# Performance work log

Hardware: AMD Instinct MI355X
Metric: run time of the kernel (lower is better)

Reference implementation:

```python
import jax, jax.numpy as jnp
import numpy as np


def setup_inputs() -> dict:
    key = jax.random.key(0)
    ks = jax.random.split(key, 8)
    C = 128
    Cq = C // 8  # 16
    x = jax.random.normal(ks[0], (4, C, 64, 64), dtype=jnp.float32)
    s = 1.0 / np.sqrt(C)
    wq = jax.random.normal(ks[1], (Cq, C), dtype=jnp.float32) * s
    bq = jnp.zeros((Cq,), dtype=jnp.float32)
    wk = jax.random.normal(ks[2], (Cq, C), dtype=jnp.float32) * s
    bk = jnp.zeros((Cq,), dtype=jnp.float32)
    wv = jax.random.normal(ks[3], (C, C), dtype=jnp.float32) * s
    bv = jnp.zeros((C,), dtype=jnp.float32)
    gamma = jnp.array([0.5], dtype=jnp.float32)
    return {"x": x, "wq": wq, "bq": bq, "wk": wk, "bk": bk,
            "wv": wv, "bv": bv, "gamma": gamma}


def reference(x, wq, bq, wk, bk, wv, bv, gamma):
    B, C, W, H = x.shape
    N = W * H
    xf = x.reshape(B, C, N)  # flatten spatial; 1x1 conv == channel matmul
    q = jnp.einsum('qc,bcn->bnq', wq, xf) + bq[None, None, :]  # B,N,Cq
    k = jnp.einsum('qc,bcn->bqn', wk, xf) + bk[None, :, None]  # B,Cq,N
    v = jnp.einsum('vc,bcn->bvn', wv, xf) + bv[None, :, None]  # B,C,N
    energy = jnp.einsum('bnq,bqm->bnm', q, k)                  # B,N,N (no scaling)
    attention = jax.nn.softmax(energy, axis=-1)
    out = jnp.einsum('bvm,bnm->bvn', v, attention)             # V @ A^T
    out = out.reshape(B, C, W, H)
    return gamma[0] * out + x
```

## Files before the change

### kernel.cpp

```cpp
#include <hip/hip_runtime.h>

#define B_    4
#define C_    128
#define CQ_   16
#define N_    4096
#define KVBLK 64

typedef short          s16x8 __attribute__((ext_vector_type(8)));
typedef unsigned short u16x4 __attribute__((ext_vector_type(4)));
typedef unsigned int   u32x4 __attribute__((ext_vector_type(4)));
typedef float          f32x4 __attribute__((ext_vector_type(4)));
typedef unsigned short u16;
typedef unsigned int   u32;

__device__ __forceinline__ u16 f2bf(float f) {
    unsigned int u = __builtin_bit_cast(unsigned int, f);
    u += 0x7fffu + ((u >> 16) & 1u);
    return (u16)(u >> 16);
}
__device__ __forceinline__ float bf2f(u16 h) {
    unsigned int u = ((unsigned int)h) << 16;
    return __builtin_bit_cast(float, u);
}
__device__ __forceinline__ s16x8 ld8bf(const u16* p) {
    return *reinterpret_cast<const s16x8*>(p);
}
__device__ __forceinline__ u32 cvtpk_bf16(float lo, float hi) {
    u32 r;
    asm("v_cvt_pk_bf16_f32 %0, %1, %2" : "=v"(r) : "v"(lo), "v"(hi));
    return r;
}
__device__ __forceinline__ void gld_lds16(const u16* src, u16* lds) {
    __builtin_amdgcn_global_load_lds(
        (const __attribute__((address_space(1))) void*)src,
        (__attribute__((address_space(3))) void*)lds, 16, 0, 0);
}

__global__ __launch_bounds__(256) void proj_all_kernel(
    const float* __restrict__ x,
    const float* __restrict__ wq, const float* __restrict__ bq,
    const float* __restrict__ wk, const float* __restrict__ bk,
    const float* __restrict__ wv, const float* __restrict__ bv,
    u16* __restrict__ Qb, u16* __restrict__ Kb, u16* __restrict__ Vb)
{
    __shared__ float smem[12800];
    const int tid = threadIdx.x;
    const int b   = blockIdx.y;
    const int nl  = tid & 63;
    const int n   = blockIdx.x * 64 + nl;
    const int ch  = tid >> 6;
    const float* xp = x + ((size_t)b * C_) * N_ + n;

    if (blockIdx.z == 0) {
        float* wqs = smem;
        float* wks = smem + 2048;
        float (*part)[4][64][17] = (float (*)[4][64][17])(smem + 4096);
        for (int i = tid; i < CQ_ * C_; i += 256) { wqs[i] = wq[i]; wks[i] = wk[i]; }
        __syncthreads();

        float qa[CQ_], ka[CQ_];
#pragma unroll
        for (int j = 0; j < CQ_; ++j) { qa[j] = 0.f; ka[j] = 0.f; }
        const int c0 = ch * 32;
        for (int c = c0; c < c0 + 32; ++c) {
            const float xv = xp[(size_t)c * N_];
#pragma unroll
            for (int j = 0; j < CQ_; ++j) {
                qa[j] = fmaf(wqs[j * C_ + c], xv, qa[j]);
                ka[j] = fmaf(wks[j * C_ + c], xv, ka[j]);
            }
        }
#pragma unroll
        for (int j = 0; j < CQ_; ++j) { part[0][ch][nl][j] = qa[j]; part[1][ch][nl][j] = ka[j]; }
        __syncthreads();

        if (tid < 128) {
            const int which = tid >> 6;
            const int n2 = tid & 63;
            const float* bias = which ? bk : bq;
            alignas(16) u16 row[32];
#pragma unroll
            for (int j = 0; j < CQ_; ++j) {
                float v = part[which][0][n2][j] + part[which][1][n2][j]
                        + part[which][2][n2][j] + part[which][3][n2][j] + bias[j];
                u16 h = f2bf(v);
                row[j]       = h;
                row[CQ_ + j] = f2bf(v - bf2f(h));
            }
            u16* dst = (which ? Kb : Qb) + ((size_t)(b * N_ + blockIdx.x * 64 + n2)) * 32;
#pragma unroll
            for (int i = 0; i < 4; ++i)
                reinterpret_cast<uint4*>(dst)[i] = reinterpret_cast<const uint4*>(row)[i];
        }
    } else {
        const int cv0 = (blockIdx.z - 1) * 32;
        float* wvs = smem;
        float (*part)[64][33] = (float (*)[64][33])(smem + 4096);
        for (int i = tid; i < 32 * C_; i += 256) wvs[i] = wv[cv0 * C_ + i];
        __syncthreads();

        float acc[32];
#pragma unroll
        for (int j = 0; j < 32; ++j) acc[j] = 0.f;
        const int c0 = ch * 32;
        for (int c = c0; c < c0 + 32; ++c) {
            const float xv = xp[(size_t)c * N_];
#pragma unroll
            for (int j = 0; j < 32; ++j) acc[j] = fmaf(wvs[j * C_ + c], xv, acc[j]);
        }
#pragma unroll
        for (int j = 0; j < 32; ++j) part[ch][nl][j] = acc[j];
        __syncthreads();

        const int jq = tid >> 6;
#pragma unroll
        for (int jj = 0; jj < 8; ++jj) {
            const int j = jq * 8 + jj;
            float v = part[0][nl][j] + part[1][nl][j] + part[2][nl][j] + part[3][nl][j]
                    + bv[cv0 + j];
            Vb[((size_t)(b * C_ + cv0 + j)) * N_ + blockIdx.x * 64 + nl] = f2bf(v);
        }
    }
}

template<int NSPLIT>
__global__ __launch_bounds__(256, 2) void attn_split_kernel(
    const u16* __restrict__ Qb, const u16* __restrict__ Kb, const u16* __restrict__ Vb,
    u16* __restrict__ Opart, float* __restrict__ Lpart)
{
    constexpr int MPER = N_ / NSPLIT;
    constexpr int NT   = MPER / KVBLK;

    __shared__ __align__(16) u16 Kt[2][KVBLK * 32];
    __shared__ __align__(16) u16 Vt[2][C_ * KVBLK];

    const int tid  = threadIdx.x;
    const int lane = tid & 63;
    const int l16  = lane & 15;
    const int g    = lane >> 4;
    const int wave = tid >> 6;
    const int b    = blockIdx.y;
    const int n0   = blockIdx.x * 128;
    const int s    = blockIdx.z;
    const int ms   = s * MPER;

    const int qn = n0 + wave * 32 + l16;
    const s16x8 qf0 = ld8bf(Qb + ((size_t)(b * N_ + qn)) * 32 + 8 * g);
    const s16x8 qf1 = ld8bf(Qb + ((size_t)(b * N_ + qn + 16)) * 32 + 8 * g);

    const int kv_s   = tid >> 2;
    const int kcol_s = ((tid & 3) * 16) ^ ((kv_s & 3) << 4);
    const u16* ksrc0 = Kb + ((size_t)b * N_ + kv_s) * 32 + (kcol_s >> 1);
    const int vc_s   = tid >> 3;
    const u16* vsrc0[4];
#pragma unroll
    for (int i = 0; i < 4; ++i) {
        const int c_i  = i * 32 + vc_s;
        const int vcol = ((tid & 7) * 16) ^ ((c_i & 7) << 4);
        vsrc0[i] = Vb + ((size_t)(b * C_ + c_i)) * N_ + (vcol >> 1);
    }

    const int kswz  = (l16 & 3) << 4;
    const int vswz  = (l16 & 7) << 4;
    const int koff1 = l16 * 32 + (((16 * (g & 1)) ^ kswz) >> 1);
    const int koff2 = l16 * 32 + (((32 + 16 * g) ^ kswz) >> 1);
    const int voffA = l16 * 64 + (((16 * g) ^ vswz) >> 1);
    const int voffB = l16 * 64 + (((64 + 16 * g) ^ vswz) >> 1);

    const bool hig = (g >= 2);
    const bool mid = (g == 1) || (g == 2);

    f32x4 acc0[8], acc1[8];
#pragma unroll
    for (int cg = 0; cg < 8; ++cg) { acc0[cg] = {}; acc1[cg] = {}; }
    float lp0 = 0.f, lp1 = 0.f;

    auto relayout = [&](const float (&p)[4][4], int ss) -> s16x8 {
        const u32 a0 = cvtpk_bf16(p[2 * ss][0],     p[2 * ss][1]);
        const u32 b0 = cvtpk_bf16(p[2 * ss][2],     p[2 * ss][3]);
        const u32 a1 = cvtpk_bf16(p[2 * ss + 1][0], p[2 * ss + 1][1]);
        const u32 b1 = cvtpk_bf16(p[2 * ss + 1][2], p[2 * ss + 1][3]);
        const u32 mA = (u32)__shfl_xor((int)(hig ? a0 : a1), 32);
        const u32 mB = (u32)__shfl_xor((int)(hig ? b0 : b1), 32);
        const u32 oA = hig ? a1 : a0;
        const u32 oB = hig ? b1 : b0;
        const u32 eA = mid ? mA : oA;
        const u32 eB = mid ? mB : oB;
        const u32 vA = mid ? oA : mA;
        const u32 vB = mid ? oB : mB;
        const u32 xA = (u32)__shfl_xor((int)vA, 16);
        const u32 xB = (u32)__shfl_xor((int)vB, 16);
        u32x4 w;
        w[0] = (g & 1) ? xA : eA;
        w[1] = (g & 1) ? xB : eB;
        w[2] = (g & 1) ? eA : xA;
        w[3] = (g & 1) ? eB : xB;
        return __builtin_bit_cast(s16x8, w);
    };

    auto body = [&](int t, int buf) {
        if (t + 1 < NT) {
            const int mn = ms + (t + 1) * KVBLK;
            gld_lds16(ksrc0 + (size_t)mn * 32, &Kt[buf ^ 1][wave * 512]);
#pragma unroll
            for (int i = 0; i < 4; ++i)
                gld_lds16(vsrc0[i] + mn, &Vt[buf ^ 1][i * 2048 + wave * 512]);
        }
        const u16* ktb = &Kt[buf][0];
        const u16* vtb = &Vt[buf][0];

        f32x4 s0[4], s1[4];
        __builtin_amdgcn_s_setprio(1);
#pragma unroll
        for (int mg = 0; mg < 4; ++mg) {
            const s16x8 kf1 = ld8bf(ktb + koff1 + mg * 512);
            s16x8 kf2 = {};
            if (g < 2) kf2 = ld8bf(ktb + koff2 + mg * 512);
            f32x4 z0 = {}, z1 = {};
            z0 = __builtin_amdgcn_mfma_f32_16x16x32_bf16(kf1, qf0, z0, 0, 0, 0);
            z0 = __builtin_amdgcn_mfma_f32_16x16x32_bf16(kf2, qf0, z0, 0, 0, 0);
            z1 = __builtin_amdgcn_mfma_f32_16x16x32_bf16(kf1, qf1, z1, 0, 0, 0);
            z1 = __builtin_amdgcn_mfma_f32_16x16x32_bf16(kf2, qf1, z1, 0, 0, 0);
            s0[mg] = z0; s1[mg] = z1;
        }
        __builtin_amdgcn_s_setprio(0);

        s16x8 pf00, pf01, pf10, pf11;
        {
            float p[4][4];
#pragma unroll
            for (int mg = 0; mg < 4; ++mg)
#pragma unroll
                for (int i = 0; i < 4; ++i) { p[mg][i] = __expf(s0[mg][i]); lp0 += p[mg][i]; }
            pf00 = relayout(p, 0); pf01 = relayout(p, 1);
        }
        {
            float p[4][4];
#pragma unroll
            for (int mg = 0; mg < 4; ++mg)
#pragma unroll
                for (int i = 0; i < 4; ++i) { p[mg][i] = __expf(s1[mg][i]); lp1 += p[mg][i]; }
            pf10 = relayout(p, 0); pf11 = relayout(p, 1);
        }

        __builtin_amdgcn_s_setprio(1);
#pragma unroll
        for (int cg = 0; cg < 8; ++cg) {
            const s16x8 vfa = ld8bf(vtb + voffA + cg * 1024);
            acc0[cg] = __builtin_amdgcn_mfma_f32_16x16x32_bf16(vfa, pf00, acc0[cg], 0, 0, 0);
            acc1[cg] = __builtin_amdgcn_mfma_f32_16x16x32_bf16(vfa, pf10, acc1[cg], 0, 0, 0);
            const s16x8 vfb = ld8bf(vtb + voffB + cg * 1024);
            acc0[cg] = __builtin_amdgcn_mfma_f32_16x16x32_bf16(vfb, pf01, acc0[cg], 0, 0, 0);
            acc1[cg] = __builtin_amdgcn_mfma_f32_16x16x32_bf16(vfb, pf11, acc1[cg], 0, 0, 0);
        }
        __builtin_amdgcn_s_setprio(0);

        asm volatile("s_waitcnt vmcnt(0)" ::: "memory");
        __syncthreads();
    };

    gld_lds16(ksrc0 + (size_t)ms * 32, &Kt[0][wave * 512]);
#pragma unroll
    for (int i = 0; i < 4; ++i)
        gld_lds16(vsrc0[i] + ms, &Vt[0][i * 2048 + wave * 512]);
    asm volatile("s_waitcnt vmcnt(0)" ::: "memory");
    __syncthreads();

    for (int tt = 0; tt < NT / 2; ++tt) {
        body(2 * tt, 0);
        body(2 * tt + 1, 1);
    }

    lp0 += __shfl_xor(lp0, 16);  lp0 += __shfl_xor(lp0, 32);
    lp1 += __shfl_xor(lp1, 16);  lp1 += __shfl_xor(lp1, 32);
    const size_t sb = (size_t)(s * B_ + b);
    if (lane < 16) {
        Lpart[sb * N_ + n0 + wave * 32 + l16]      = lp0;
        Lpart[sb * N_ + n0 + wave * 32 + 16 + l16] = lp1;
    }

    const int na = n0 + wave * 32 + l16;
#pragma unroll
    for (int cg = 0; cg < 8; ++cg) {
#pragma unroll
        for (int i = 0; i < 4; ++i) {
            const int c = 16 * cg + 4 * g + i;
            Opart[(sb * C_ + c) * N_ + na]      = f2bf(acc0[cg][i]);
            Opart[(sb * C_ + c) * N_ + na + 16] = f2bf(acc1[cg][i]);
        }
    }
}

template<int NSPLIT>
__global__ __launch_bounds__(256) void reduce_kernel(
    const u16* __restrict__ Opart, const float* __restrict__ Lpart,
    const float* __restrict__ x, const float* __restrict__ gamma,
    float* __restrict__ out)
{
    const int t  = blockIdx.x * 256 + threadIdx.x;
    const size_t e0 = (size_t)t * 4;
    const int n = (int)(e0 & (N_ - 1));
    const int c = (int)((e0 >> 12) & (C_ - 1));
    const int b = (int)(e0 >> 19);

    float o0 = 0.f, o1 = 0.f, o2 = 0.f, o3 = 0.f;
    f32x4 l = {};
#pragma unroll
    for (int s = 0; s < NSPLIT; ++s) {
        const size_t sb = (size_t)(s * B_ + b);
        const u16x4 ov = *reinterpret_cast<const u16x4*>(Opart + (sb * C_ + c) * N_ + n);
        const f32x4 lv = *reinterpret_cast<const f32x4*>(Lpart + sb * N_ + n);
        o0 += bf2f(ov[0]); o1 += bf2f(ov[1]); o2 += bf2f(ov[2]); o3 += bf2f(ov[3]);
        l += lv;
    }
    const float gm = gamma[0];
    const f32x4 xv = *reinterpret_cast<const f32x4*>(x + e0);
    f32x4 r;
    r[0] = gm * o0 / l[0] + xv[0];
    r[1] = gm * o1 / l[1] + xv[1];
    r[2] = gm * o2 / l[2] + xv[2];
    r[3] = gm * o3 / l[3] + xv[3];
    *reinterpret_cast<f32x4*>(out + e0) = r;
}

extern "C" void kernel_launch(void* const* d_in, const int* in_sizes, int n_in,
                              void* d_out, int out_size, void* d_ws, size_t ws_size,
                              hipStream_t stream)
{
    const float* x     = (const float*)d_in[0];
    const float* wq    = (const float*)d_in[1];
    const float* bq    = (const float*)d_in[2];
    const float* wk    = (const float*)d_in[3];
    const float* bk    = (const float*)d_in[4];
    const float* wv    = (const float*)d_in[5];
    const float* bv    = (const float*)d_in[6];
    const float* gamma = (const float*)d_in[7];
    float* out = (float*)d_out;

    u16* Qb = (u16*)d_ws;
    u16* Kb = Qb + (size_t)B_ * N_ * 32;
    u16* Vb = Kb + (size_t)B_ * N_ * 32;
    u16* Opart = Vb + (size_t)B_ * C_ * N_;

    const size_t fixed = (size_t)(B_ * N_ * 32) * 2 * 2 + (size_t)(B_ * C_ * N_) * 2;
    const size_t per_split = (size_t)B_ * C_ * N_ * 2 + (size_t)B_ * N_ * 4;
    const bool use8 = ws_size >= fixed + 8 * per_split;

    proj_all_kernel<<<dim3(N_ / 64, B_, 5), 256, 0, stream>>>(
        x, wq, bq, wk, bk, wv, bv, Qb, Kb, Vb);

    if (use8) {
        float* Lpart = (float*)(Opart + (size_t)8 * B_ * C_ * N_);
        attn_split_kernel<8><<<dim3(N_ / 128, B_, 8), 256, 0, stream>>>(
            Qb, Kb, Vb, Opart, Lpart);
        reduce_kernel<8><<<(B_ * C_ * N_ / 4) / 256, 256, 0, stream>>>(
            Opart, Lpart, x, gamma, out);
    } else {
        float* Lpart = (float*)(Opart + (size_t)4 * B_ * C_ * N_);
        attn_split_kernel<4><<<dim3(N_ / 128, B_, 4), 256, 0, stream>>>(
            Qb, Kb, Vb, Opart, Lpart);
        reduce_kernel<4><<<(B_ * C_ * N_ / 4) / 256, 256, 0, stream>>>(
            Opart, Lpart, x, gamma, out);
    }
}
```

Before: 80.32 us.

## Permute V layout to drop P relayout shuffles, use exp2 and MFMA row sums

V is written with a permuted spatial order inside each 64-column block, so the P fragments from the QK MFMA can feed the PV MFMA directly without the cross-lane shuffle relayout. Q is prescaled by log2(e) so exp2f replaces __expf. Row sums now come from extra MFMAs against a ones vector, which replaces the per-lane adds and the final shuffle reductions. Occupancy is raised to 3 blocks per SM. Together these remove VALU and permute work in the softmax stage, at the cost of four extra MFMAs per tile and more register pressure from the occupancy hint.

```diff
diff --git a/kernel.cpp b/kernel.cpp
--- a/kernel.cpp
+++ b/kernel.cpp
@@ -34,6 +34,10 @@
     __builtin_amdgcn_global_load_lds(
         (const __attribute__((address_space(1))) void*)src,
         (__attribute__((address_space(3))) void*)lds, 16, 0, 0);
+}
+
+__device__ __forceinline__ int invpi64(int r) {
+    return (r & 0x23) | ((r & 0x10) >> 2) | ((r & 0x0C) << 1);
 }
 
 __global__ __launch_bounds__(256) void proj_all_kernel(
@@ -78,11 +82,12 @@
             const int which = tid >> 6;
             const int n2 = tid & 63;
             const float* bias = which ? bk : bq;
+            const float scale = which ? 1.0f : 1.4426950408889634f;
             alignas(16) u16 row[32];
 #pragma unroll
             for (int j = 0; j < CQ_; ++j) {
-                float v = part[which][0][n2][j] + part[which][1][n2][j]
-                        + part[which][2][n2][j] + part[which][3][n2][j] + bias[j];
+                float v = (part[which][0][n2][j] + part[which][1][n2][j]
+                         + part[which][2][n2][j] + part[which][3][n2][j] + bias[j]) * scale;
                 u16 h = f2bf(v);
                 row[j]       = h;
                 row[CQ_ + j] = f2bf(v - bf2f(h));
@@ -112,19 +117,20 @@
         for (int j = 0; j < 32; ++j) part[ch][nl][j] = acc[j];
         __syncthreads();
 
-        const int jq = tid >> 6;
+        const int jq  = tid >> 6;
+        const int nlp = invpi64(nl);
 #pragma unroll
         for (int jj = 0; jj < 8; ++jj) {
             const int j = jq * 8 + jj;
             float v = part[0][nl][j] + part[1][nl][j] + part[2][nl][j] + part[3][nl][j]
                     + bv[cv0 + j];
-            Vb[((size_t)(b * C_ + cv0 + j)) * N_ + blockIdx.x * 64 + nl] = f2bf(v);
+            Vb[((size_t)(b * C_ + cv0 + j)) * N_ + blockIdx.x * 64 + nlp] = f2bf(v);
         }
     }
 }
 
 template<int NSPLIT>
-__global__ __launch_bounds__(256, 2) void attn_split_kernel(
+__global__ __launch_bounds__(256, 3) void attn_split_kernel(
     const u16* __restrict__ Qb, const u16* __restrict__ Kb, const u16* __restrict__ Vb,
     u16* __restrict__ Opart, float* __restrict__ Lpart)
 {
@@ -167,34 +173,20 @@
     const int voffA = l16 * 64 + (((16 * g) ^ vswz) >> 1);
     const int voffB = l16 * 64 + (((64 + 16 * g) ^ vswz) >> 1);
 
-    const bool hig = (g >= 2);
-    const bool mid = (g == 1) || (g == 2);
+    const s16x8 ones = { 0x3F80, 0x3F80, 0x3F80, 0x3F80,
+                         0x3F80, 0x3F80, 0x3F80, 0x3F80 };
 
     f32x4 acc0[8], acc1[8];
 #pragma unroll
     for (int cg = 0; cg < 8; ++cg) { acc0[cg] = {}; acc1[cg] = {}; }
-    float lp0 = 0.f, lp1 = 0.f;
-
-    auto relayout = [&](const float (&p)[4][4], int ss) -> s16x8 {
-        const u32 a0 = cvtpk_bf16(p[2 * ss][0],     p[2 * ss][1]);
-        const u32 b0 = cvtpk_bf16(p[2 * ss][2],     p[2 * ss][3]);
-        const u32 a1 = cvtpk_bf16(p[2 * ss + 1][0], p[2 * ss + 1][1]);
-        const u32 b1 = cvtpk_bf16(p[2 * ss + 1][2], p[2 * ss + 1][3]);
-        const u32 mA = (u32)__shfl_xor((int)(hig ? a0 : a1), 32);
-        const u32 mB = (u32)__shfl_xor((int)(hig ? b0 : b1), 32);
-        const u32 oA = hig ? a1 : a0;
-        const u32 oB = hig ? b1 : b0;
-        const u32 eA = mid ? mA : oA;
-        const u32 eB = mid ? mB : oB;
-        const u32 vA = mid ? oA : mA;
-        const u32 vB = mid ? oB : mB;
-        const u32 xA = (u32)__shfl_xor((int)vA, 16);
-        const u32 xB = (u32)__shfl_xor((int)vB, 16);
+    f32x4 accl0 = {}, accl1 = {};
+
+    auto packpf = [&](const float (&p)[4][4], int ss) -> s16x8 {
         u32x4 w;
-        w[0] = (g & 1) ? xA : eA;
-        w[1] = (g & 1) ? xB : eB;
-        w[2] = (g & 1) ? eA : xA;
-        w[3] = (g & 1) ? eB : xB;
+        w[0] = cvtpk_bf16(p[2 * ss][0],     p[2 * ss][1]);
+        w[1] = cvtpk_bf16(p[2 * ss][2],     p[2 * ss][3]);
+        w[2] = cvtpk_bf16(p[2 * ss + 1][0], p[2 * ss + 1][1]);
+        w[3] = cvtpk_bf16(p[2 * ss + 1][2], p[2 * ss + 1][3]);
         return __builtin_bit_cast(s16x8, w);
     };
 
@@ -225,33 +217,37 @@
         }
         __builtin_amdgcn_s_setprio(0);
 
-        s16x8 pf00, pf01, pf10, pf11;
+        s16x8 pf0a, pf0b, pf1a, pf1b;
         {
             float p[4][4];
 #pragma unroll
             for (int mg = 0; mg < 4; ++mg)
 #pragma unroll
-                for (int i = 0; i < 4; ++i) { p[mg][i] = __expf(s0[mg][i]); lp0 += p[mg][i]; }
-            pf00 = relayout(p, 0); pf01 = relayout(p, 1);
+                for (int i = 0; i < 4; ++i) p[mg][i] = exp2f(s0[mg][i]);
+            pf0a = packpf(p, 0); pf0b = packpf(p, 1);
         }
         {
             float p[4][4];
 #pragma unroll
             for (int mg = 0; mg < 4; ++mg)
 #pragma unroll
-                for (int i = 0; i < 4; ++i) { p[mg][i] = __expf(s1[mg][i]); lp1 += p[mg][i]; }
-            pf10 = relayout(p, 0); pf11 = relayout(p, 1);
+                for (int i = 0; i < 4; ++i) p[mg][i] = exp2f(s1[mg][i]);
+            pf1a = packpf(p, 0); pf1b = packpf(p, 1);
         }
 
         __builtin_amdgcn_s_setprio(1);
+        accl0 = __builtin_amdgcn_mfma_f32_16x16x32_bf16(ones, pf0a, accl0, 0, 0, 0);
+        accl0 = __builtin_amdgcn_mfma_f32_16x16x32_bf16(ones, pf0b, accl0, 0, 0, 0);
+        accl1 = __builtin_amdgcn_mfma_f32_16x16x32_bf16(ones, pf1a, accl1, 0, 0, 0);
+        accl1 = __builtin_amdgcn_mfma_f32_16x16x32_bf16(ones, pf1b, accl1, 0, 0, 0);
 #pragma unroll
         for (int cg = 0; cg < 8; ++cg) {
             const s16x8 vfa = ld8bf(vtb + voffA + cg * 1024);
-            acc0[cg] = __builtin_amdgcn_mfma_f32_16x16x32_bf16(vfa, pf00, acc0[cg], 0, 0, 0);
-            acc1[cg] = __builtin_amdgcn_mfma_f32_16x16x32_bf16(vfa, pf10, acc1[cg], 0, 0, 0);
+            acc0[cg] = __builtin_amdgcn_mfma_f32_16x16x32_bf16(vfa, pf0a, acc0[cg], 0, 0, 0);
+            acc1[cg] = __builtin_amdgcn_mfma_f32_16x16x32_bf16(vfa, pf1a, acc1[cg], 0, 0, 0);
             const s16x8 vfb = ld8bf(vtb + voffB + cg * 1024);
-            acc0[cg] = __builtin_amdgcn_mfma_f32_16x16x32_bf16(vfb, pf01, acc0[cg], 0, 0, 0);
-            acc1[cg] = __builtin_amdgcn_mfma_f32_16x16x32_bf16(vfb, pf11, acc1[cg], 0, 0, 0);
+            acc0[cg] = __builtin_amdgcn_mfma_f32_16x16x32_bf16(vfb, pf0b, acc0[cg], 0, 0, 0);
+            acc1[cg] = __builtin_amdgcn_mfma_f32_16x16x32_bf16(vfb, pf1b, acc1[cg], 0, 0, 0);
         }
         __builtin_amdgcn_s_setprio(0);
 
@@ -271,12 +267,10 @@
         body(2 * tt + 1, 1);
     }
 
-    lp0 += __shfl_xor(lp0, 16);  lp0 += __shfl_xor(lp0, 32);
-    lp1 += __shfl_xor(lp1, 16);  lp1 += __shfl_xor(lp1, 32);
     const size_t sb = (size_t)(s * B_ + b);
     if (lane < 16) {
-        Lpart[sb * N_ + n0 + wave * 32 + l16]      = lp0;
-        Lpart[sb * N_ + n0 + wave * 32 + 16 + l16] = lp1;
+        Lpart[sb * N_ + n0 + wave * 32 + l16]      = accl0[0];
+        Lpart[sb * N_ + n0 + wave * 32 + 16 + l16] = accl1[0];
     }
 
     const int na = n0 + wave * 32 + l16;
```

Result: faster. 77.73 us (-3.2%).
